# Kernel optimization log

Measured on AMD Instinct MI355X. Metric: run time of the kernel, lower is better.

## Reference

```python
import jax, jax.numpy as jnp
import numpy as np

N, D = 16384, 256

def setup_inputs() -> dict:
    key = jax.random.key(0)
    k1, k2 = jax.random.split(key)
    image_emb = jax.random.normal(k1, (N, D), dtype=jnp.float32)
    text_emb = jax.random.normal(k2, (N, D), dtype=jnp.float32)
    return {"image_emb": image_emb, "text_emb": text_emb}

def reference(image_emb, text_emb):
    n = image_emb.shape[0]
    # [n, n] similarity logits
    logits = image_emb @ text_emb.T
    labels = jnp.arange(n)
    # cross-entropy with diagonal labels: -log_softmax(logits)[i, i]
    logp_t = jax.nn.log_softmax(logits, axis=-1)        # image -> text (rows)
    logp_i = jax.nn.log_softmax(logits.T, axis=-1)      # text -> image (cols)
    loss_t = -logp_t[labels, labels]
    loss_i = -logp_i[labels, labels]
    loss = ((loss_i + loss_t) * 0.5).mean()
    return loss
```

## Files before the change

### kernel.cpp

```cpp
#include <hip/hip_runtime.h>
#include <hip/hip_bf16.h>

#define NN 16384
#define DD 256

typedef unsigned short u16;
typedef unsigned int u32;
typedef unsigned char u8;
typedef long i64;
typedef __attribute__((ext_vector_type(4))) float f32x4;
typedef __attribute__((ext_vector_type(4))) int i32x4;
typedef __attribute__((ext_vector_type(8))) int i32x8;

__global__ __launch_bounds__(256) void prep_kernel(
        const float* __restrict__ img, const float* __restrict__ txt,
        u8* __restrict__ A8, u8* __restrict__ B8,
        float* __restrict__ zbuf ,
        float* __restrict__ out) {
    __shared__ u32 sA[16 * 65 + 8];
    __shared__ u32 sB[16 * 65 + 8];
    const int t = threadIdx.x, bi = blockIdx.x;
    const float4* ib = (const float4*)img + ((size_t)bi << 10);
    const float4* tb = (const float4*)txt + ((size_t)bi << 10);
    const float S = 1.44269504088896f;
    #pragma unroll
    for (int k = 0; k < 4; ++k) {
        const int idx = (k << 8) + t;
        const int row = idx >> 6, col = idx & 63;
        float4 va = ib[idx];
        int pa = __builtin_amdgcn_cvt_pk_fp8_f32(va.x * S, va.y * S, 0, false);
        pa     = __builtin_amdgcn_cvt_pk_fp8_f32(va.z * S, va.w * S, pa, true);
        sA[row * 65 + col] = (u32)pa;
        float4 vb = tb[idx];
        int pb = __builtin_amdgcn_cvt_pk_fp8_f32(vb.x, vb.y, 0, false);
        pb     = __builtin_amdgcn_cvt_pk_fp8_f32(vb.z, vb.w, pb, true);
        sB[row * 65 + col] = (u32)pb;
    }
    __syncthreads();
    const int w = t >> 6, l = t & 63;
    const int k2 = w >> 1, jj = w & 1, qq = l >> 4, mm = l & 15;
    const int wb = mm * 65 + (k2 << 5) + (qq << 3) + (jj << 2);
    i32x4 oa = { (int)sA[wb], (int)sA[wb + 1], (int)sA[wb + 2], (int)sA[wb + 3] };
    i32x4 ob = { (int)sB[wb], (int)sB[wb + 1], (int)sB[wb + 2], (int)sB[wb + 3] };
    const size_t dst = ((size_t)(bi >> 3) << 15) + (k2 << 14) + ((size_t)(bi & 7) << 11)
                     + (jj << 10) + (qq << 8) + (mm << 4);
    *(i32x4*)(A8 + dst) = oa;
    *(i32x4*)(B8 + dst) = ob;
    const int gid = (bi << 8) + t;
    if (gid < 32768) zbuf[gid] = 0.0f;
    if (gid == 0) out[0] = 0.0f;
}

__global__ __launch_bounds__(256, 2) void gemm_lse_kernel(
        const u8* __restrict__ A8, const u8* __restrict__ B8,
        float* __restrict__ s_row, float* __restrict__ s_col,
        float* __restrict__ diag) {
    const int t = threadIdx.x;
    const int lane = t & 63;
    const int w = t >> 6;
    const int wr = w >> 1, wc = w & 1;
    const int q = lane >> 4, m = lane & 15;
    const int bi = blockIdx.x & 127;
    const int jg = blockIdx.x >> 7;
    const int row0 = bi << 7;

    const u8* Aw = A8 + ((size_t)bi << 15) + ((size_t)lane << 4);
    i32x8 areg[2][4];
    #pragma unroll
    for (int k2 = 0; k2 < 2; ++k2)
        #pragma unroll
        for (int rb = 0; rb < 4; ++rb) {
            const u8* p = Aw + (k2 << 14) + (((wr << 2) + rb) << 11);
            i32x4 lo = *(const i32x4*)(p);
            i32x4 hi = *(const i32x4*)(p + 1024);
            areg[k2][rb] = __builtin_shufflevector(lo, hi, 0, 1, 2, 3, 4, 5, 6, 7);
        }

    const f32x4 fzero = {0.f, 0.f, 0.f, 0.f};
    f32x4 accA[4][2], accB[4][2];
    f32x4 rp[4] = {fzero, fzero, fzero, fzero};
    float cpartT = 0.0f;

    const u8* Bw = B8 + (wc << 13) + ((size_t)lane << 4);

    auto mfma_half = [&](f32x4 (&acc)[4][2], int jt_, int h) {
        const int ct = (jg << 4) | ((jt_ + bi) & 15);
        const u8* p = Bw + ((size_t)ct << 15) + (h << 12);
        const f32x4 cinit = {-144.f, -144.f, -144.f, -144.f};
        #pragma unroll
        for (int k2 = 0; k2 < 2; ++k2) {
            const u8* pp = p + (k2 << 14);
            i32x4 lo0 = *(const i32x4*)(pp);
            i32x4 hi0 = *(const i32x4*)(pp + 1024);
            i32x8 bf0 = __builtin_shufflevector(lo0, hi0, 0, 1, 2, 3, 4, 5, 6, 7);
            i32x4 lo1 = *(const i32x4*)(pp + 2048);
            i32x4 hi1 = *(const i32x4*)(pp + 3072);
            i32x8 bf1 = __builtin_shufflevector(lo1, hi1, 0, 1, 2, 3, 4, 5, 6, 7);
            if (k2 == 0) {
                #pragma unroll
                for (int rb = 0; rb < 4; ++rb) {
                    acc[rb][0] = __builtin_amdgcn_mfma_scale_f32_16x16x128_f8f6f4(
                        areg[0][rb], bf0, cinit, 0, 0, 0, 127, 0, 127);
                    acc[rb][1] = __builtin_amdgcn_mfma_scale_f32_16x16x128_f8f6f4(
                        areg[0][rb], bf1, cinit, 0, 0, 0, 127, 0, 127);
                }
            } else {
                #pragma unroll
                for (int rb = 0; rb < 4; ++rb) {
                    acc[rb][0] = __builtin_amdgcn_mfma_scale_f32_16x16x128_f8f6f4(
                        areg[1][rb], bf0, acc[rb][0], 0, 0, 0, 127, 0, 127);
                    acc[rb][1] = __builtin_amdgcn_mfma_scale_f32_16x16x128_f8f6f4(
                        areg[1][rb], bf1, acc[rb][1], 0, 0, 0, 127, 0, 127);
                }
            }
        }
    };

    auto epilogue_half = [&](f32x4 (&acc)[4][2], int jt_, int h) {
        const int ct = (jg << 4) | ((jt_ + bi) & 15);
        if (bi == ct && wr == wc) {
            #pragma unroll
            for (int rb = 0; rb < 4; ++rb)
                if ((rb >> 1) == h) {
                    #pragma unroll
                    for (int r = 0; r < 4; ++r)
                        if (m == ((q << 2) | r))
                            diag[row0 + (wr << 6) + (rb << 4) + m] = acc[rb][rb & 1][r];
                }
        }
        #pragma unroll
        for (int rb = 0; rb < 4; ++rb)
            #pragma unroll
            for (int cb = 0; cb < 2; ++cb)
                #pragma unroll
                for (int r = 0; r < 4; ++r)
                    acc[rb][cb][r] = __builtin_amdgcn_exp2f(acc[rb][cb][r]);
        #pragma unroll
        for (int rb = 0; rb < 4; ++rb)
            rp[rb] += acc[rb][0] + acc[rb][1];
        #pragma unroll
        for (int cb = 0; cb < 2; ++cb) {
            f32x4 s = (acc[0][cb] + acc[1][cb]) + (acc[2][cb] + acc[3][cb]);
            float v = (s[0] + s[1]) + (s[2] + s[3]);
            v += __shfl_xor(v, 16, 64);
            v += __shfl_xor(v, 32, 64);
            if (q == ((h << 1) | cb)) cpartT = v;
        }
        if (h == 1) {
            const int col0 = ct << 7;
            atomicAdd(&s_col[col0 + (wc << 6) + (q << 4) + m], cpartT);
        }
    };

    mfma_half(accA, 0, 0);
    #pragma unroll 1
    for (int jt = 0; jt < 15; ++jt) {
        mfma_half(accB, jt, 1);
        epilogue_half(accA, jt, 0);
        mfma_half(accA, jt + 1, 0);
        epilogue_half(accB, jt, 1);
    }
    mfma_half(accB, 15, 1);
    epilogue_half(accA, 15, 0);
    epilogue_half(accB, 15, 1);

    float rout = 0.0f;
    #pragma unroll
    for (int rb = 0; rb < 4; ++rb)
        #pragma unroll
        for (int r = 0; r < 4; ++r) {
            float v = rp[rb][r];
            v += __shfl_xor(v, 1, 16);
            v += __shfl_xor(v, 2, 16);
            v += __shfl_xor(v, 4, 16);
            v += __shfl_xor(v, 8, 16);
            if (m == ((rb << 2) | r)) rout = v;
        }
    atomicAdd(&s_row[row0 + (wr << 6) + ((m >> 2) << 4) + (q << 2) + (m & 3)], rout);
}

__global__ void final_kernel(const float* __restrict__ s_row, const float* __restrict__ s_col,
                             const float* __restrict__ diag, float* __restrict__ out) {
    __shared__ double red[256];
    int t = threadIdx.x;
    int i = blockIdx.x * 256 + t;
    double p = 0.5 * (double)(log2f(s_row[i]) + log2f(s_col[i])) - (double)diag[i];
    red[t] = p;
    __syncthreads();
    for (int s = 128; s > 0; s >>= 1) {
        if (t < s) red[t] += red[t + s];
        __syncthreads();
    }
    if (t == 0) atomicAdd(out, (float)(red[0] * 0.6931471805599453 / (double)NN));
}

extern "C" void kernel_launch(void* const* d_in, const int* in_sizes, int n_in,
                              void* d_out, int out_size, void* d_ws, size_t ws_size,
                              hipStream_t stream) {
    const float* img = (const float*)d_in[0];
    const float* txt = (const float*)d_in[1];
    char* ws = (char*)d_ws;
    u8*    A8    = (u8*)ws;
    u8*    B8    = (u8*)(ws + 4194304);
    float* s_row = (float*)(ws + 8388608);
    float* s_col = (float*)(ws + 8388608 + 65536);
    float* diag  = (float*)(ws + 8388608 + 131072);
    float* out   = (float*)d_out;

    prep_kernel<<<1024, 256, 0, stream>>>(img, txt, A8, B8, s_row, out);
    gemm_lse_kernel<<<1024, 256, 0, stream>>>(A8, B8, s_row, s_col, diag);
    final_kernel<<<64, 256, 0, stream>>>(s_row, s_col, diag, out);
}
```

Baseline: 144.7 us.

## Split GEMM-LSE block into eight waves with 32-row wave tiles

Doubles the GEMM+logsumexp block to 512 threads (eight waves), so each wave owns 32 rows by 64 columns instead of 64 by 64. This halves the A-fragment registers, accumulators and row partials per wave, and the launch bounds now request four blocks per CU, aiming for more resident waves to hide load and exp latency. The diagonal extraction and row-sum atomics are reindexed for the new wave layout. In exchange, every wave still loads the full B fragments for its columns while issuing half as many MFMAs per load, so B traffic per MFMA doubles.

After: 188.8 us. 30.6% more time.

```diff
diff --git a/kernel.cpp b/kernel.cpp
--- a/kernel.cpp
+++ b/kernel.cpp
@@ -51,7 +51,7 @@
     if (gid == 0) out[0] = 0.0f;
 }
 
-__global__ __launch_bounds__(256, 2) void gemm_lse_kernel(
+__global__ __launch_bounds__(512, 4) void gemm_lse_kernel(
         const u8* __restrict__ A8, const u8* __restrict__ B8,
         float* __restrict__ s_row, float* __restrict__ s_col,
         float* __restrict__ diag) {
@@ -65,82 +65,83 @@
     const int row0 = bi << 7;
 
     const u8* Aw = A8 + ((size_t)bi << 15) + ((size_t)lane << 4);
-    i32x8 areg[2][4];
+    i32x8 areg[2][2];
     #pragma unroll
     for (int k2 = 0; k2 < 2; ++k2)
         #pragma unroll
-        for (int rb = 0; rb < 4; ++rb) {
-            const u8* p = Aw + (k2 << 14) + (((wr << 2) + rb) << 11);
+        for (int rb = 0; rb < 2; ++rb) {
+            const u8* p = Aw + (k2 << 14) + (((wr << 1) + rb) << 11);
             i32x4 lo = *(const i32x4*)(p);
             i32x4 hi = *(const i32x4*)(p + 1024);
             areg[k2][rb] = __builtin_shufflevector(lo, hi, 0, 1, 2, 3, 4, 5, 6, 7);
         }
 
     const f32x4 fzero = {0.f, 0.f, 0.f, 0.f};
-    f32x4 accA[4][2], accB[4][2];
-    f32x4 rp[4] = {fzero, fzero, fzero, fzero};
+    f32x4 accA[2][2], accB[2][2];
+    f32x4 rp[2] = {fzero, fzero};
     float cpartT = 0.0f;
 
     const u8* Bw = B8 + (wc << 13) + ((size_t)lane << 4);
 
-    auto mfma_half = [&](f32x4 (&acc)[4][2], int jt_, int h) {
+    auto mfma_half = [&](f32x4 (&acc)[2][2], int jt_, int h) {
         const int ct = (jg << 4) | ((jt_ + bi) & 15);
         const u8* p = Bw + ((size_t)ct << 15) + (h << 12);
         const f32x4 cinit = {-144.f, -144.f, -144.f, -144.f};
+        i32x8 bf[4];
         #pragma unroll
         for (int k2 = 0; k2 < 2; ++k2) {
             const u8* pp = p + (k2 << 14);
             i32x4 lo0 = *(const i32x4*)(pp);
             i32x4 hi0 = *(const i32x4*)(pp + 1024);
-            i32x8 bf0 = __builtin_shufflevector(lo0, hi0, 0, 1, 2, 3, 4, 5, 6, 7);
+            bf[k2 * 2 + 0] = __builtin_shufflevector(lo0, hi0, 0, 1, 2, 3, 4, 5, 6, 7);
             i32x4 lo1 = *(const i32x4*)(pp + 2048);
             i32x4 hi1 = *(const i32x4*)(pp + 3072);
-            i32x8 bf1 = __builtin_shufflevector(lo1, hi1, 0, 1, 2, 3, 4, 5, 6, 7);
-            if (k2 == 0) {
-                #pragma unroll
-                for (int rb = 0; rb < 4; ++rb) {
-                    acc[rb][0] = __builtin_amdgcn_mfma_scale_f32_16x16x128_f8f6f4(
-                        areg[0][rb], bf0, cinit, 0, 0, 0, 127, 0, 127);
-                    acc[rb][1] = __builtin_amdgcn_mfma_scale_f32_16x16x128_f8f6f4(
-                        areg[0][rb], bf1, cinit, 0, 0, 0, 127, 0, 127);
-                }
-            } else {
-                #pragma unroll
-                for (int rb = 0; rb < 4; ++rb) {
-                    acc[rb][0] = __builtin_amdgcn_mfma_scale_f32_16x16x128_f8f6f4(
-                        areg[1][rb], bf0, acc[rb][0], 0, 0, 0, 127, 0, 127);
-                    acc[rb][1] = __builtin_amdgcn_mfma_scale_f32_16x16x128_f8f6f4(
-                        areg[1][rb], bf1, acc[rb][1], 0, 0, 0, 127, 0, 127);
-                }
-            }
+            bf[k2 * 2 + 1] = __builtin_shufflevector(lo1, hi1, 0, 1, 2, 3, 4, 5, 6, 7);
+        }
+        #pragma unroll
+        for (int rb = 0; rb < 2; ++rb) {
+            acc[rb][0] = __builtin_amdgcn_mfma_scale_f32_16x16x128_f8f6f4(
+                areg[0][rb], bf[0], cinit, 0, 0, 0, 127, 0, 127);
+            acc[rb][1] = __builtin_amdgcn_mfma_scale_f32_16x16x128_f8f6f4(
+                areg[0][rb], bf[1], cinit, 0, 0, 0, 127, 0, 127);
+        }
+        #pragma unroll
+        for (int rb = 0; rb < 2; ++rb) {
+            acc[rb][0] = __builtin_amdgcn_mfma_scale_f32_16x16x128_f8f6f4(
+                areg[1][rb], bf[2], acc[rb][0], 0, 0, 0, 127, 0, 127);
+            acc[rb][1] = __builtin_amdgcn_mfma_scale_f32_16x16x128_f8f6f4(
+                areg[1][rb], bf[3], acc[rb][1], 0, 0, 0, 127, 0, 127);
         }
     };
 
-    auto epilogue_half = [&](f32x4 (&acc)[4][2], int jt_, int h) {
+    auto epilogue_half = [&](f32x4 (&acc)[2][2], int jt_, int h) {
         const int ct = (jg << 4) | ((jt_ + bi) & 15);
-        if (bi == ct && wr == wc) {
+        if (bi == ct) {
             #pragma unroll
-            for (int rb = 0; rb < 4; ++rb)
-                if ((rb >> 1) == h) {
+            for (int rb = 0; rb < 2; ++rb) {
+                const int dj = (wr << 1) + rb;
+                if ((dj >> 2) == wc && (((dj >> 1) & 1) == h)) {
+                    const int cbl = dj & 1;
                     #pragma unroll
                     for (int r = 0; r < 4; ++r)
                         if (m == ((q << 2) | r))
-                            diag[row0 + (wr << 6) + (rb << 4) + m] = acc[rb][rb & 1][r];
+                            diag[row0 + (wr << 5) + (rb << 4) + m] = acc[rb][cbl][r];
                 }
-        }
-        #pragma unroll
-        for (int rb = 0; rb < 4; ++rb)
+            }
+        }
+        #pragma unroll
+        for (int rb = 0; rb < 2; ++rb)
             #pragma unroll
             for (int cb = 0; cb < 2; ++cb)
                 #pragma unroll
                 for (int r = 0; r < 4; ++r)
                     acc[rb][cb][r] = __builtin_amdgcn_exp2f(acc[rb][cb][r]);
         #pragma unroll
-        for (int rb = 0; rb < 4; ++rb)
+        for (int rb = 0; rb < 2; ++rb)
             rp[rb] += acc[rb][0] + acc[rb][1];
         #pragma unroll
         for (int cb = 0; cb < 2; ++cb) {
-            f32x4 s = (acc[0][cb] + acc[1][cb]) + (acc[2][cb] + acc[3][cb]);
+            f32x4 s = acc[0][cb] + acc[1][cb];
             float v = (s[0] + s[1]) + (s[2] + s[3]);
             v += __shfl_xor(v, 16, 64);
             v += __shfl_xor(v, 32, 64);
@@ -166,7 +167,7 @@
 
     float rout = 0.0f;
     #pragma unroll
-    for (int rb = 0; rb < 4; ++rb)
+    for (int rb = 0; rb < 2; ++rb)
         #pragma unroll
         for (int r = 0; r < 4; ++r) {
             float v = rp[rb][r];
@@ -176,7 +177,8 @@
             v += __shfl_xor(v, 8, 16);
             if (m == ((rb << 2) | r)) rout = v;
         }
-    atomicAdd(&s_row[row0 + (wr << 6) + ((m >> 2) << 4) + (q << 2) + (m & 3)], rout);
+    if (m < 8)
+        atomicAdd(&s_row[row0 + (wr << 5) + ((m >> 2) << 4) + (q << 2) + (m & 3)], rout);
 }
 
 __global__ void final_kernel(const float* __restrict__ s_row, const float* __restrict__ s_col,
@@ -208,6 +210,6 @@
     float* out   = (float*)d_out;
 
     prep_kernel<<<1024, 256, 0, stream>>>(img, txt, A8, B8, s_row, out);
-    gemm_lse_kernel<<<1024, 256, 0, stream>>>(A8, B8, s_row, s_col, diag);
+    gemm_lse_kernel<<<1024, 512, 0, stream>>>(A8, B8, s_row, s_col, diag);
     final_kernel<<<64, 256, 0, stream>>>(s_row, s_col, diag, out);
 }
```

## Software-pipeline B-fragment loads with rotating register banks across MFMA slots

Applied to the files above, without the earlier changes.

Splits each half-tile's B loads into eight slot loads held in four rotating register banks, so each global load is issued one or two MFMA groups before it is consumed, including prefetching the next tile's first slots. The main loop is restructured to interleave these loads with MFMAs and the epilogues of the previous halves. This aims to hide global/L2 load latency behind matrix ops, at the cost of more live vector registers, which could pressure occupancy at the two-blocks-per-SIMD launch bound.

Measured after the change: 145.1 us. About the same (+0.3%).

```diff
diff --git a/kernel.cpp b/kernel.cpp
--- a/kernel.cpp
+++ b/kernel.cpp
@@ -83,36 +83,29 @@
 
     const u8* Bw = B8 + (wc << 13) + ((size_t)lane << 4);
 
-    auto mfma_half = [&](f32x4 (&acc)[4][2], int jt_, int h) {
+    i32x8 bf0, bf1, bf2, bf3;
+
+    auto load_slot = [&](i32x8& bank, int jt_, int ii) {
         const int ct = (jg << 4) | ((jt_ + bi) & 15);
-        const u8* p = Bw + ((size_t)ct << 15) + (h << 12);
+        const u8* pp = Bw + ((size_t)ct << 15) + ((ii >> 2) << 12)
+                     + (((ii >> 1) & 1) << 14) + ((ii & 1) << 11);
+        i32x4 lo = *(const i32x4*)(pp);
+        i32x4 hi = *(const i32x4*)(pp + 1024);
+        bank = __builtin_shufflevector(lo, hi, 0, 1, 2, 3, 4, 5, 6, 7);
+    };
+
+    auto mfma_slot = [&](f32x4 (&acc)[4][2], const i32x8& bank, int k2_, int cbl_) {
         const f32x4 cinit = {-144.f, -144.f, -144.f, -144.f};
-        #pragma unroll
-        for (int k2 = 0; k2 < 2; ++k2) {
-            const u8* pp = p + (k2 << 14);
-            i32x4 lo0 = *(const i32x4*)(pp);
-            i32x4 hi0 = *(const i32x4*)(pp + 1024);
-            i32x8 bf0 = __builtin_shufflevector(lo0, hi0, 0, 1, 2, 3, 4, 5, 6, 7);
-            i32x4 lo1 = *(const i32x4*)(pp + 2048);
-            i32x4 hi1 = *(const i32x4*)(pp + 3072);
-            i32x8 bf1 = __builtin_shufflevector(lo1, hi1, 0, 1, 2, 3, 4, 5, 6, 7);
-            if (k2 == 0) {
-                #pragma unroll
-                for (int rb = 0; rb < 4; ++rb) {
-                    acc[rb][0] = __builtin_amdgcn_mfma_scale_f32_16x16x128_f8f6f4(
-                        areg[0][rb], bf0, cinit, 0, 0, 0, 127, 0, 127);
-                    acc[rb][1] = __builtin_amdgcn_mfma_scale_f32_16x16x128_f8f6f4(
-                        areg[0][rb], bf1, cinit, 0, 0, 0, 127, 0, 127);
-                }
-            } else {
-                #pragma unroll
-                for (int rb = 0; rb < 4; ++rb) {
-                    acc[rb][0] = __builtin_amdgcn_mfma_scale_f32_16x16x128_f8f6f4(
-                        areg[1][rb], bf0, acc[rb][0], 0, 0, 0, 127, 0, 127);
-                    acc[rb][1] = __builtin_amdgcn_mfma_scale_f32_16x16x128_f8f6f4(
-                        areg[1][rb], bf1, acc[rb][1], 0, 0, 0, 127, 0, 127);
-                }
-            }
+        if (k2_ == 0) {
+            #pragma unroll
+            for (int rb = 0; rb < 4; ++rb)
+                acc[rb][cbl_] = __builtin_amdgcn_mfma_scale_f32_16x16x128_f8f6f4(
+                    areg[0][rb], bank, cinit, 0, 0, 0, 127, 0, 127);
+        } else {
+            #pragma unroll
+            for (int rb = 0; rb < 4; ++rb)
+                acc[rb][cbl_] = __builtin_amdgcn_mfma_scale_f32_16x16x128_f8f6f4(
+                    areg[1][rb], bank, acc[rb][cbl_], 0, 0, 0, 127, 0, 127);
         }
     };
 
@@ -152,16 +145,23 @@
         }
     };
 
-    mfma_half(accA, 0, 0);
+    load_slot(bf0, 0, 0);
+    load_slot(bf1, 0, 1);
     #pragma unroll 1
-    for (int jt = 0; jt < 15; ++jt) {
-        mfma_half(accB, jt, 1);
+    for (int jt = 0; jt < 16; ++jt) {
+        load_slot(bf2, jt, 2);  mfma_slot(accA, bf0, 0, 0);
+        load_slot(bf3, jt, 3);  mfma_slot(accA, bf1, 0, 1);
+        load_slot(bf0, jt, 4);  mfma_slot(accA, bf2, 1, 0);
+        load_slot(bf1, jt, 5);  mfma_slot(accA, bf3, 1, 1);
+        if (jt > 0) epilogue_half(accB, jt - 1, 1);
+        load_slot(bf2, jt, 6);  mfma_slot(accB, bf0, 0, 0);
+        load_slot(bf3, jt, 7);  mfma_slot(accB, bf1, 0, 1);
+        if (jt < 15) load_slot(bf0, jt + 1, 0);
+        mfma_slot(accB, bf2, 1, 0);
+        if (jt < 15) load_slot(bf1, jt + 1, 1);
+        mfma_slot(accB, bf3, 1, 1);
         epilogue_half(accA, jt, 0);
-        mfma_half(accA, jt + 1, 0);
-        epilogue_half(accB, jt, 1);
     }
-    mfma_half(accB, 15, 1);
-    epilogue_half(accA, 15, 0);
     epilogue_half(accB, 15, 1);
 
     float rout = 0.0f;
```
